# Optimization experiments

Measured on AMD Instinct MI355X. Metric: run time of the kernel, lower is better.

The kernel has to match this reference:

```python
import jax, jax.numpy as jnp
import numpy as np

N_HEAD = 16
D_MODEL = 1024
BATCH = 2
SEQ = 2048


def setup_inputs() -> dict:
    key = jax.random.key(0)
    ks = jax.random.split(key, 12)
    s = 0.02
    inp = {
        "q": jax.random.normal(ks[0], (BATCH, SEQ, D_MODEL), jnp.float32),
        "k": jax.random.normal(ks[1], (BATCH, SEQ, D_MODEL), jnp.float32),
        "v": jax.random.normal(ks[2], (BATCH, SEQ, D_MODEL), jnp.float32),
        "Wq": jax.random.normal(ks[3], (D_MODEL, D_MODEL), jnp.float32) * s,
        "bq": jnp.zeros((D_MODEL,), jnp.float32),
        "Wk": jax.random.normal(ks[4], (D_MODEL, D_MODEL), jnp.float32) * s,
        "bk": jnp.zeros((D_MODEL,), jnp.float32),
        "Wv": jax.random.normal(ks[5], (D_MODEL, D_MODEL), jnp.float32) * s,
        "bv": jnp.zeros((D_MODEL,), jnp.float32),
        "Wo": jax.random.normal(ks[6], (D_MODEL, D_MODEL), jnp.float32) * s,
        "bo": jnp.zeros((D_MODEL,), jnp.float32),
    }
    return inp


def reference(q, k, v, Wq, bq, Wk, bk, Wv, bv, Wo, bo):
    B, S, D = q.shape
    H = N_HEAD
    Dh = D // H
    # NOTE: faithful to source -- scale uses d_model, not head_dim
    scale = D ** 0.5

    # torch nn.Linear: y = x @ W.T + b
    qw = q @ Wq.T + bq
    kw = k @ Wk.T + bk
    vw = v @ Wv.T + bv

    # chunk(n_head, dim=-1) == contiguous last-dim head slices
    qh = qw.reshape(B, S, H, Dh)
    kh = kw.reshape(B, S, H, Dh)
    vh = vw.reshape(B, S, H, Dh)

    scores = jnp.einsum("bshd,bthd->bhst", qh, kh) / scale  # [B,H,S,S]
    causal = jnp.triu(jnp.ones((S, S), dtype=bool), k=1)
    scores = jnp.where(causal, -jnp.inf, scores)
    p = jax.nn.softmax(scores, axis=-1)
    out = jnp.einsum("bhst,bthd->bshd", p, vh).reshape(B, S, D)
    return out @ Wo.T + bo
```

## Files before the change

kernel.cpp:

```cpp
#include <hip/hip_runtime.h>
#include <hip/hip_bf16.h>
#include <stdint.h>
#include <type_traits>

#define NHEAD  16
#define DMODEL 1024
#define BATCH  2
#define SEQ    2048
#define DH     64
#define MROWS  (BATCH*SEQ)

typedef __attribute__((ext_vector_type(8))) short bf16x8;
typedef __attribute__((ext_vector_type(4))) float f32x4;

__device__ inline short f2bs(float f) {
    __hip_bfloat16 h = __float2bfloat16(f);
    return *reinterpret_cast<short*>(&h);
}

__device__ inline uint32_t pk2f(float lo, float hi) {
    uint32_t ul, uh;
    __builtin_memcpy(&ul, &lo, 4);
    __builtin_memcpy(&uh, &hi, 4);
    return __builtin_amdgcn_perm(uh + 0x8000u, ul + 0x8000u, 0x07060302u);
}

__device__ inline void async16(const void* g, void* l) {
    __builtin_amdgcn_global_load_lds(
        (__attribute__((address_space(1))) void*)g,
        (__attribute__((address_space(3))) void*)l, 16, 0, 0);
}

__global__ __launch_bounds__(256)
void convert_all(const float* __restrict__ Wq, const float* __restrict__ Wk,
                 const float* __restrict__ Wv, const float* __restrict__ Wo,
                 const float* __restrict__ q, const float* __restrict__ k,
                 const float* __restrict__ v,
                 __hip_bfloat16* __restrict__ Wqkv, __hip_bfloat16* __restrict__ Wob,
                 __hip_bfloat16* __restrict__ qb, __hip_bfloat16* __restrict__ kb,
                 __hip_bfloat16* __restrict__ vb)
{
    const int idx = (blockIdx.x * 256 + threadIdx.x) * 8;
    const float* src;
    __hip_bfloat16* dst;
    if (idx < 3 * 1048576) {
        const int g = idx >> 20;
        src = (g == 0 ? Wq : (g == 1 ? Wk : Wv)) + (idx & 1048575);
        dst = Wqkv + idx;
    } else if (idx < 4 * 1048576) {
        src = Wo + (idx - 3 * 1048576);
        dst = Wob + (idx - 3 * 1048576);
    } else if (idx < 8 * 1048576) {
        src = q + (idx - 4 * 1048576);
        dst = qb + (idx - 4 * 1048576);
    } else if (idx < 12 * 1048576) {
        src = k + (idx - 8 * 1048576);
        dst = kb + (idx - 8 * 1048576);
    } else {
        src = v + (idx - 12 * 1048576);
        dst = vb + (idx - 12 * 1048576);
    }
    float4 f0 = *(const float4*)src;
    float4 f1 = *(const float4*)(src + 4);
    short o[8];
    o[0] = f2bs(f0.x); o[1] = f2bs(f0.y); o[2] = f2bs(f0.z); o[3] = f2bs(f0.w);
    o[4] = f2bs(f1.x); o[5] = f2bs(f1.y); o[6] = f2bs(f1.z); o[7] = f2bs(f1.w);
    *(uint4*)dst = *(uint4*)o;
}

template <typename TC, bool DBUF, bool VTOUT>
__global__ __launch_bounds__(256, DBUF ? 2 : 3)
void gemm_bt(const __hip_bfloat16* __restrict__ A0, const __hip_bfloat16* __restrict__ A1,
             const __hip_bfloat16* __restrict__ A2,
             const __hip_bfloat16* __restrict__ B,
             const float* __restrict__ b0, const float* __restrict__ b1, const float* __restrict__ b2,
             TC* __restrict__ C0, TC* __restrict__ C1, TC* __restrict__ C2,
             float os0)
{
    __shared__ short As[DBUF ? 2 : 1][128 * 64];
    __shared__ short Bs[DBUF ? 2 : 1][128 * 64];

    const int t    = threadIdx.x;
    const int lane = t & 63;
    const int w    = t >> 6;
    const int wm   = (w >> 1) * 64;
    const int wn   = (w & 1) * 64;
    const int quad = lane >> 4;
    const int l16  = lane & 15;

    const int g = blockIdx.x >> 3;
    const __hip_bfloat16* A = (g == 0) ? A0 : (g == 1 ? A1 : A2);
    const float* bias       = (g == 0) ? b0 : (g == 1 ? b1 : b2);
    TC* C                   = (g == 0) ? C0 : (g == 1 ? C1 : C2);
    const float osc         = (g == 0) ? os0 : 1.f;
    const int    bm  = blockIdx.y * 128;
    const int    bnl = (blockIdx.x & 7) * 128;
    const size_t bng = (size_t)blockIdx.x * 128;

    f32x4 acc[4][4];
#pragma unroll
    for (int i = 0; i < 4; i++)
#pragma unroll
        for (int j = 0; j < 4; j++)
            acc[i][j] = (f32x4){0.f, 0.f, 0.f, 0.f};

    auto STAGEG = [&](int kt, int buf) {
#pragma unroll
        for (int i = 0; i < 4; i++) {
            const int p  = i * 256 + t;
            const int br = p >> 3;
            const int c8 = ((p & 7) - br) & 7;
            async16(B + (bng + br) * DMODEL + kt + c8 * 8,
                    &Bs[buf][(i * 256 + (w << 6)) * 8]);
            async16(A + (size_t)(bm + br) * DMODEL + kt + c8 * 8,
                    &As[buf][(i * 256 + (w << 6)) * 8]);
        }
    };

    int cur = 0;
    if constexpr (DBUF) STAGEG(0, 0);

    for (int kt = 0; kt < DMODEL; kt += 64) {
        __syncthreads();
        if constexpr (DBUF) {
            if (kt + 64 < DMODEL) STAGEG(kt + 64, cur ^ 1);
        } else {
            STAGEG(kt, 0);
            __syncthreads();
        }

#pragma unroll
        for (int kk = 0; kk < 2; kk++) {
            bf16x8 af[4], bf[4];
#pragma unroll
            for (int mi = 0; mi < 4; mi++) {
                const int row = wm + mi * 16 + l16;
                const int pc  = ((quad + 4 * kk) + row) & 7;
                af[mi] = *(const bf16x8*)&As[cur][row * 64 + pc * 8];
            }
#pragma unroll
            for (int ni = 0; ni < 4; ni++) {
                const int row = wn + ni * 16 + l16;
                const int pc  = ((quad + 4 * kk) + row) & 7;
                bf[ni] = *(const bf16x8*)&Bs[cur][row * 64 + pc * 8];
            }
#pragma unroll
            for (int mi = 0; mi < 4; mi++)
#pragma unroll
                for (int ni = 0; ni < 4; ni++)
                    acc[mi][ni] = __builtin_amdgcn_mfma_f32_16x16x32_bf16(
                        af[mi], bf[ni], acc[mi][ni], 0, 0, 0);
        }
        if constexpr (DBUF) cur ^= 1;
    }

#pragma unroll
    for (int mi = 0; mi < 4; mi++) {
#pragma unroll
        for (int ni = 0; ni < 4; ni++) {
            const int row0 = bm + wm + mi * 16 + quad * 4;
            const int coll = bnl + wn + ni * 16 + l16;
            const float bb = bias[coll];
            if (VTOUT && g == 2) {
                const int hh = coll >> 6, dd = coll & 63;
                const int bb_ = row0 >> 11, s0 = row0 & 2047;
                short o4[4];
#pragma unroll
                for (int r = 0; r < 4; r++) o4[r] = f2bs(acc[mi][ni][r] + bb);
                __hip_bfloat16* dst = (__hip_bfloat16*)C2 +
                    ((size_t)((bb_ * NHEAD + hh) * DH + dd)) * SEQ + s0;
                *(uint2*)dst = *(uint2*)o4;
            } else {
#pragma unroll
                for (int r = 0; r < 4; r++) {
                    const float val = (acc[mi][ni][r] + bb) * osc;
                    if constexpr (std::is_same<TC, float>::value)
                        C[(size_t)(row0 + r) * DMODEL + coll] = val;
                    else
                        C[(size_t)(row0 + r) * DMODEL + coll] = __float2bfloat16(val);
                }
            }
        }
    }
}

__global__ __launch_bounds__(256, 5)
void attn_flash_wg(const __hip_bfloat16* __restrict__ qp,
                   const __hip_bfloat16* __restrict__ kp,
                   const __hip_bfloat16* __restrict__ vt,
                   __hip_bfloat16* __restrict__ ao)
{
    __shared__ short Ks[2][64 * 64];
    __shared__ short Vs[2][64 * 64];

    const int t    = threadIdx.x;
    const int lane = t & 63;
    const int w    = t >> 6;
    const int l16  = lane & 15;
    const int quad = lane >> 4;

    const int bh = blockIdx.x & 31;
    const int p  = blockIdx.x >> 5;
    const int pa = p & 7, pb = p >> 3;
    const int st = (pb == 0) ? pa : (pb == 1) ? 15 - pa
                 : (pb == 2) ? 16 + pa : 31 - pa;
    const int b = bh >> 4;
    const int h = bh & 15;

    const __hip_bfloat16* qptr =
        qp + (size_t)(b * SEQ + 64 * st + 16 * w + l16) * DMODEL + h * DH + quad * 8;
    bf16x8 aq0 = *(const bf16x8*)qptr;
    bf16x8 aq1 = *(const bf16x8*)(qptr + 32);

    float l = 0.f;
    f32x4 oc[4];
#pragma unroll
    for (int dt = 0; dt < 4; dt++) oc[dt] = (f32x4){0.f, 0.f, 0.f, 0.f};

    const __hip_bfloat16* kbase = kp + (size_t)(b * SEQ) * DMODEL + h * DH;
    const __hip_bfloat16* vbase = vt + (size_t)(bh * DH) * SEQ;

    const int nst = st + 1;
    const int rql = 16 * w + l16;

    const int p1  = 256 + t;
    const int r0s = t >> 3,            r1s = p1 >> 3;
    const int c80 = ((t & 7) - r0s) & 7, c81 = ((p1 & 7) - r1s) & 7;
    const int kr0 = (r0s & 3) | ((r0s & 12) << 1) | ((r0s & 16) << 1) | ((r0s & 32) >> 3);
    const int kr1 = (r1s & 3) | ((r1s & 12) << 1) | ((r1s & 16) << 1) | ((r1s & 32) >> 3);
    const __hip_bfloat16* ks0 = kbase + (size_t)kr0 * DMODEL + c80 * 8;
    const __hip_bfloat16* ks1 = kbase + (size_t)kr1 * DMODEL + c81 * 8;
    const __hip_bfloat16* vs0 = vbase + (size_t)r0s * SEQ + c80 * 8;
    const __hip_bfloat16* vs1 = vbase + (size_t)r1s * SEQ + c81 * 8;

    const int d0 = ((w << 6)) * 8;
    const int d1 = (256 + (w << 6)) * 8;

    async16(ks0, &Ks[0][d0]);
    async16(ks1, &Ks[0][d1]);
    async16(vs0, &Vs[0][d0]);
    async16(vs1, &Vs[0][d1]);
    int cur = 0;
    int key0 = 0;

    for (int js = 0; js < nst; ++js) {
        __syncthreads();
        if (js + 1 < nst) {
            ks0 += (size_t)64 * DMODEL;  ks1 += (size_t)64 * DMODEL;
            vs0 += 64;                   vs1 += 64;
            const int nb = cur ^ 1;
            async16(ks0, &Ks[nb][d0]);
            async16(ks1, &Ks[nb][d1]);
            async16(vs0, &Vs[nb][d0]);
            async16(vs1, &Vs[nb][d1]);
        }

        f32x4 sc[4];
        __builtin_amdgcn_s_setprio(1);
#pragma unroll
        for (int ct = 0; ct < 4; ct++) {
            const int row = 16 * ct + l16;
            bf16x8 bk0 = *(const bf16x8*)&Ks[cur][row * 64 + ((quad + row) & 7) * 8];
            bf16x8 bk1 = *(const bf16x8*)&Ks[cur][row * 64 + ((quad + 4 + row) & 7) * 8];
            sc[ct] = __builtin_amdgcn_mfma_f32_16x16x32_bf16(
                bk0, aq0, (f32x4){0.f, 0.f, 0.f, 0.f}, 0, 0, 0);
            sc[ct] = __builtin_amdgcn_mfma_f32_16x16x32_bf16(bk1, aq1, sc[ct], 0, 0, 0);
        }
        __builtin_amdgcn_s_setprio(0);

        if (key0 == 64 * st) {
#pragma unroll
            for (int ct = 0; ct < 4; ct++)
#pragma unroll
                for (int r = 0; r < 4; r++) {
                    const int km = 8 * quad + 32 * (ct & 1) + 4 * (ct >> 1) + r;
                    if (km > rql) sc[ct][r] = -__builtin_inff();
                }
        }

        float psum = 0.f;
#pragma unroll
        for (int ct = 0; ct < 4; ct++)
#pragma unroll
            for (int r = 0; r < 4; r++) {
                const float e = exp2f(sc[ct][r]);
                sc[ct][r] = e;
                psum += e;
            }

        union U8 { uint32_t u[4]; bf16x8 v; } ap0u, ap1u;
        ap0u.u[0] = pk2f(sc[0][0], sc[0][1]);
        ap0u.u[1] = pk2f(sc[0][2], sc[0][3]);
        ap0u.u[2] = pk2f(sc[2][0], sc[2][1]);
        ap0u.u[3] = pk2f(sc[2][2], sc[2][3]);
        ap1u.u[0] = pk2f(sc[1][0], sc[1][1]);
        ap1u.u[1] = pk2f(sc[1][2], sc[1][3]);
        ap1u.u[2] = pk2f(sc[3][0], sc[3][1]);
        ap1u.u[3] = pk2f(sc[3][2], sc[3][3]);

        __builtin_amdgcn_s_setprio(1);
#pragma unroll
        for (int dt = 0; dt < 4; dt++) {
            const int row = 16 * dt + l16;
            bf16x8 bv0 = *(const bf16x8*)&Vs[cur][row * 64 + ((quad + row) & 7) * 8];
            bf16x8 bv1 = *(const bf16x8*)&Vs[cur][row * 64 + ((quad + 4 + row) & 7) * 8];
            oc[dt] = __builtin_amdgcn_mfma_f32_16x16x32_bf16(ap0u.v, bv0, oc[dt], 0, 0, 0);
            oc[dt] = __builtin_amdgcn_mfma_f32_16x16x32_bf16(ap1u.v, bv1, oc[dt], 0, 0, 0);
        }
        __builtin_amdgcn_s_setprio(0);

        psum += __shfl_xor(psum, 16);
        psum += __shfl_xor(psum, 32);
        l += psum;
        key0 += 64;
        cur ^= 1;
    }

    __hip_bfloat16* aobase = ao + (size_t)(b * SEQ + 64 * st + 16 * w) * DMODEL + h * DH;
#pragma unroll
    for (int r = 0; r < 4; r++) {
        const float lr  = __shfl(l, quad * 4 + r);
        const float inv = 1.f / lr;
        const int   row = quad * 4 + r;
#pragma unroll
        for (int dt = 0; dt < 4; dt++)
            aobase[(size_t)row * DMODEL + 16 * dt + l16] = __float2bfloat16(oc[dt][r] * inv);
    }
}

extern "C" void kernel_launch(void* const* d_in, const int* in_sizes, int n_in,
                              void* d_out, int out_size, void* d_ws, size_t ws_size,
                              hipStream_t stream) {
    const float* q  = (const float*)d_in[0];
    const float* k  = (const float*)d_in[1];
    const float* v  = (const float*)d_in[2];
    const float* Wq = (const float*)d_in[3];
    const float* bq = (const float*)d_in[4];
    const float* Wk = (const float*)d_in[5];
    const float* bk = (const float*)d_in[6];
    const float* Wv = (const float*)d_in[7];
    const float* bv = (const float*)d_in[8];
    const float* Wo = (const float*)d_in[9];
    const float* bo = (const float*)d_in[10];
    float* out = (float*)d_out;

    __hip_bfloat16* Wqkv = (__hip_bfloat16*)d_ws;
    __hip_bfloat16* Wob  = Wqkv + (size_t)3072 * 1024;
    __hip_bfloat16* qp   = Wob  + (size_t)1024 * 1024;
    __hip_bfloat16* kp   = qp   + (size_t)MROWS * DMODEL;
    __hip_bfloat16* vtg  = kp   + (size_t)MROWS * DMODEL;
    __hip_bfloat16* vb   = vtg  + (size_t)MROWS * DMODEL;
    __hip_bfloat16* qb   = (__hip_bfloat16*)d_out;
    __hip_bfloat16* kb   = qb + (size_t)MROWS * DMODEL;
    __hip_bfloat16* ao   = vb;

    const float qscale = 0.03125f * 1.44269504088896340736f;

    hipLaunchKernelGGL(convert_all, dim3(8192), dim3(256), 0, stream,
                       Wq, Wk, Wv, Wo, q, k, v, Wqkv, Wob, qb, kb, vb);

    hipLaunchKernelGGL((gemm_bt<__hip_bfloat16, false, true>), dim3(24, 32), dim3(256), 0, stream,
                       qb, kb, vb, Wqkv, bq, bk, bv, qp, kp, vtg, qscale);

    hipLaunchKernelGGL(attn_flash_wg, dim3(1024), dim3(256), 0, stream,
                       qp, kp, vtg, ao);

    hipLaunchKernelGGL((gemm_bt<float, true, false>), dim3(8, 32), dim3(256), 0, stream,
                       ao, ao, ao, Wob, bo, bo, bo, out, out, out, 1.0f);
}
```

Before: 211.3 us.

## Split long causal attention tiles across two blocks and add reduce kernel

Query tiles 16-31 of the causal attention now have their key range split in half across two workgroups. A static ordering table schedules the heaviest pieces first, and each split half writes unnormalized bf16 partial outputs plus row sums into scratch. A new attn_reduce2 kernel then combines the two halves and normalizes them. This balances load across the grid and shortens the tail of the longest tiles, at the cost of an extra launch and extra partial-result traffic. Separately, the fp32 output GEMM swaps its MFMA operands so each lane can store four contiguous columns as float4 with a vectorized bias load.

Result: no change. 208.4 us (-1.4%).

```diff
diff --git a/kernel.cpp b/kernel.cpp
--- a/kernel.cpp
+++ b/kernel.cpp
@@ -23,6 +23,13 @@
     __builtin_memcpy(&ul, &lo, 4);
     __builtin_memcpy(&uh, &hi, 4);
     return __builtin_amdgcn_perm(uh + 0x8000u, ul + 0x8000u, 0x07060302u);
+}
+
+__device__ inline float bs2f(short s) {
+    const uint32_t u = (uint32_t)(uint16_t)s << 16;
+    float f;
+    __builtin_memcpy(&f, &u, 4);
+    return f;
 }
 
 __device__ inline void async16(const void* g, void* l) {
@@ -77,6 +84,7 @@
              TC* __restrict__ C0, TC* __restrict__ C1, TC* __restrict__ C2,
              float os0)
 {
+    constexpr bool SWAPC = std::is_same<TC, float>::value;
     __shared__ short As[DBUF ? 2 : 1][128 * 64];
     __shared__ short Bs[DBUF ? 2 : 1][128 * 64];
 
@@ -147,9 +155,14 @@
 #pragma unroll
             for (int mi = 0; mi < 4; mi++)
 #pragma unroll
-                for (int ni = 0; ni < 4; ni++)
-                    acc[mi][ni] = __builtin_amdgcn_mfma_f32_16x16x32_bf16(
-                        af[mi], bf[ni], acc[mi][ni], 0, 0, 0);
+                for (int ni = 0; ni < 4; ni++) {
+                    if constexpr (SWAPC)
+                        acc[mi][ni] = __builtin_amdgcn_mfma_f32_16x16x32_bf16(
+                            bf[ni], af[mi], acc[mi][ni], 0, 0, 0);
+                    else
+                        acc[mi][ni] = __builtin_amdgcn_mfma_f32_16x16x32_bf16(
+                            af[mi], bf[ni], acc[mi][ni], 0, 0, 0);
+                }
         }
         if constexpr (DBUF) cur ^= 1;
     }
@@ -158,26 +171,35 @@
     for (int mi = 0; mi < 4; mi++) {
 #pragma unroll
         for (int ni = 0; ni < 4; ni++) {
-            const int row0 = bm + wm + mi * 16 + quad * 4;
-            const int coll = bnl + wn + ni * 16 + l16;
-            const float bb = bias[coll];
-            if (VTOUT && g == 2) {
-                const int hh = coll >> 6, dd = coll & 63;
-                const int bb_ = row0 >> 11, s0 = row0 & 2047;
-                short o4[4];
-#pragma unroll
-                for (int r = 0; r < 4; r++) o4[r] = f2bs(acc[mi][ni][r] + bb);
-                __hip_bfloat16* dst = (__hip_bfloat16*)C2 +
-                    ((size_t)((bb_ * NHEAD + hh) * DH + dd)) * SEQ + s0;
-                *(uint2*)dst = *(uint2*)o4;
+            if constexpr (SWAPC) {
+                const int m  = bm + wm + mi * 16 + l16;
+                const int nb = bnl + wn + ni * 16 + quad * 4;
+                const float4 b4 = *(const float4*)&bias[nb];
+                float4 o;
+                o.x = acc[mi][ni][0] + b4.x;
+                o.y = acc[mi][ni][1] + b4.y;
+                o.z = acc[mi][ni][2] + b4.z;
+                o.w = acc[mi][ni][3] + b4.w;
+                *(float4*)&C[(size_t)m * DMODEL + nb] = o;
             } else {
-#pragma unroll
-                for (int r = 0; r < 4; r++) {
-                    const float val = (acc[mi][ni][r] + bb) * osc;
-                    if constexpr (std::is_same<TC, float>::value)
-                        C[(size_t)(row0 + r) * DMODEL + coll] = val;
-                    else
+                const int row0 = bm + wm + mi * 16 + quad * 4;
+                const int coll = bnl + wn + ni * 16 + l16;
+                const float bb = bias[coll];
+                if (VTOUT && g == 2) {
+                    const int hh = coll >> 6, dd = coll & 63;
+                    const int bb_ = row0 >> 11, s0 = row0 & 2047;
+                    short o4[4];
+#pragma unroll
+                    for (int r = 0; r < 4; r++) o4[r] = f2bs(acc[mi][ni][r] + bb);
+                    __hip_bfloat16* dst = (__hip_bfloat16*)C2 +
+                        ((size_t)((bb_ * NHEAD + hh) * DH + dd)) * SEQ + s0;
+                    *(uint2*)dst = *(uint2*)o4;
+                } else {
+#pragma unroll
+                    for (int r = 0; r < 4; r++) {
+                        const float val = (acc[mi][ni][r] + bb) * osc;
                         C[(size_t)(row0 + r) * DMODEL + coll] = __float2bfloat16(val);
+                    }
                 }
             }
         }
@@ -188,8 +210,23 @@
 void attn_flash_wg(const __hip_bfloat16* __restrict__ qp,
                    const __hip_bfloat16* __restrict__ kp,
                    const __hip_bfloat16* __restrict__ vt,
-                   __hip_bfloat16* __restrict__ ao)
+                   __hip_bfloat16* __restrict__ ao,
+                   __hip_bfloat16* __restrict__ po,
+                   float* __restrict__ ml)
 {
+    static const unsigned char ord[48] = {
+        62, 63, 60, 15,
+        61, 58, 59, 56, 14,
+        57, 54, 55, 52, 13,
+        53, 50, 51, 48, 12,
+        49, 46, 47, 44, 11,
+        45, 42, 43, 40, 10,
+        41, 38, 39, 36,  9,
+        37, 34, 35, 32,  8,
+        33,  7,
+         6,  5,  4,  3,  2,  1,  0
+    };
+
     __shared__ short Ks[2][64 * 64];
     __shared__ short Vs[2][64 * 64];
 
@@ -200,10 +237,20 @@
     const int quad = lane >> 4;
 
     const int bh = blockIdx.x & 31;
-    const int p  = blockIdx.x >> 5;
-    const int pa = p & 7, pb = p >> 3;
-    const int st = (pb == 0) ? pa : (pb == 1) ? 15 - pa
-                 : (pb == 2) ? 16 + pa : 31 - pa;
+    const int u  = blockIdx.x >> 5;
+    const int v  = ord[u];
+    int st, js0, nst;
+    bool split;
+    if (v >= 32) {
+        st = v >> 1;
+        const int S  = st + 1;
+        const int h0 = (S + 1) >> 1;
+        if ((v & 1) == 0) { js0 = 0;  nst = h0; }
+        else              { js0 = h0; nst = S - h0; }
+        split = true;
+    } else {
+        st = v; js0 = 0; nst = st + 1; split = false;
+    }
     const int b = bh >> 4;
     const int h = bh & 15;
 
@@ -220,7 +267,6 @@
     const __hip_bfloat16* kbase = kp + (size_t)(b * SEQ) * DMODEL + h * DH;
     const __hip_bfloat16* vbase = vt + (size_t)(bh * DH) * SEQ;
 
-    const int nst = st + 1;
     const int rql = 16 * w + l16;
 
     const int p1  = 256 + t;
@@ -228,10 +274,11 @@
     const int c80 = ((t & 7) - r0s) & 7, c81 = ((p1 & 7) - r1s) & 7;
     const int kr0 = (r0s & 3) | ((r0s & 12) << 1) | ((r0s & 16) << 1) | ((r0s & 32) >> 3);
     const int kr1 = (r1s & 3) | ((r1s & 12) << 1) | ((r1s & 16) << 1) | ((r1s & 32) >> 3);
-    const __hip_bfloat16* ks0 = kbase + (size_t)kr0 * DMODEL + c80 * 8;
-    const __hip_bfloat16* ks1 = kbase + (size_t)kr1 * DMODEL + c81 * 8;
-    const __hip_bfloat16* vs0 = vbase + (size_t)r0s * SEQ + c80 * 8;
-    const __hip_bfloat16* vs1 = vbase + (size_t)r1s * SEQ + c81 * 8;
+    const int kofs = js0 * 64;
+    const __hip_bfloat16* ks0 = kbase + (size_t)(kofs + kr0) * DMODEL + c80 * 8;
+    const __hip_bfloat16* ks1 = kbase + (size_t)(kofs + kr1) * DMODEL + c81 * 8;
+    const __hip_bfloat16* vs0 = vbase + (size_t)r0s * SEQ + kofs + c80 * 8;
+    const __hip_bfloat16* vs1 = vbase + (size_t)r1s * SEQ + kofs + c81 * 8;
 
     const int d0 = ((w << 6)) * 8;
     const int d1 = (256 + (w << 6)) * 8;
@@ -241,7 +288,7 @@
     async16(vs0, &Vs[0][d0]);
     async16(vs1, &Vs[0][d1]);
     int cur = 0;
-    int key0 = 0;
+    int key0 = kofs;
 
     for (int js = 0; js < nst; ++js) {
         __syncthreads();
@@ -316,16 +363,59 @@
         cur ^= 1;
     }
 
-    __hip_bfloat16* aobase = ao + (size_t)(b * SEQ + 64 * st + 16 * w) * DMODEL + h * DH;
-#pragma unroll
-    for (int r = 0; r < 4; r++) {
-        const float lr  = __shfl(l, quad * 4 + r);
-        const float inv = 1.f / lr;
-        const int   row = quad * 4 + r;
-#pragma unroll
-        for (int dt = 0; dt < 4; dt++)
-            aobase[(size_t)row * DMODEL + 16 * dt + l16] = __float2bfloat16(oc[dt][r] * inv);
-    }
+    if (!split) {
+        __hip_bfloat16* aobase = ao + (size_t)(b * SEQ + 64 * st + 16 * w) * DMODEL + h * DH;
+#pragma unroll
+        for (int r = 0; r < 4; r++) {
+            const float lr  = __shfl(l, quad * 4 + r);
+            const float inv = 1.f / lr;
+            const int   row = quad * 4 + r;
+#pragma unroll
+            for (int dt = 0; dt < 4; dt++)
+                aobase[(size_t)row * DMODEL + 16 * dt + l16] =
+                    __float2bfloat16(oc[dt][r] * inv);
+        }
+    } else {
+        const int bid = ((v - 32) << 5) | bh;
+        __hip_bfloat16* pp = po + (size_t)bid * 4096;
+#pragma unroll
+        for (int r = 0; r < 4; r++) {
+            const int row = 16 * w + quad * 4 + r;
+#pragma unroll
+            for (int dt = 0; dt < 4; dt++)
+                pp[row * 64 + 16 * dt + l16] = __float2bfloat16(oc[dt][r]);
+        }
+        if (quad == 0)
+            ml[(size_t)bid * 64 + 16 * w + l16] = l;
+    }
+}
+
+__global__ __launch_bounds__(256)
+void attn_reduce2(const __hip_bfloat16* __restrict__ po, const float* __restrict__ ml,
+                  __hip_bfloat16* __restrict__ ao)
+{
+    const int t   = threadIdx.x;
+    const int rh  = blockIdx.x & 1;
+    const int bh  = (blockIdx.x >> 1) & 31;
+    const int k   = blockIdx.x >> 6;
+    const int st  = 16 + k;
+    const int bidA = ((2 * k) << 5) | bh;
+    const int bidB = ((2 * k + 1) << 5) | bh;
+    const int b   = bh >> 4;
+    const int h   = bh & 15;
+    const int row = rh * 32 + (t >> 3);
+    const int colg = (t & 7) * 8;
+
+    const float L = ml[(size_t)bidA * 64 + row] + ml[(size_t)bidB * 64 + row];
+    union { uint4 u; short s[8]; } pa, pb;
+    pa.u = *(const uint4*)&po[(size_t)bidA * 4096 + row * 64 + colg];
+    pb.u = *(const uint4*)&po[(size_t)bidB * 4096 + row * 64 + colg];
+    const float inv = 1.f / L;
+    short o8[8];
+#pragma unroll
+    for (int j = 0; j < 8; j++)
+        o8[j] = f2bs((bs2f(pa.s[j]) + bs2f(pb.s[j])) * inv);
+    *(uint4*)&ao[(size_t)(b * SEQ + 64 * st + row) * DMODEL + h * DH + colg] = *(uint4*)o8;
 }
 
 extern "C" void kernel_launch(void* const* d_in, const int* in_sizes, int n_in,
@@ -350,9 +440,11 @@
     __hip_bfloat16* kp   = qp   + (size_t)MROWS * DMODEL;
     __hip_bfloat16* vtg  = kp   + (size_t)MROWS * DMODEL;
     __hip_bfloat16* vb   = vtg  + (size_t)MROWS * DMODEL;
+    float*          mlb  = (float*)(vb + (size_t)MROWS * DMODEL);
     __hip_bfloat16* qb   = (__hip_bfloat16*)d_out;
     __hip_bfloat16* kb   = qb + (size_t)MROWS * DMODEL;
     __hip_bfloat16* ao   = vb;
+    __hip_bfloat16* po   = (__hip_bfloat16*)d_out;
 
     const float qscale = 0.03125f * 1.44269504088896340736f;
 
@@ -362,8 +454,11 @@
     hipLaunchKernelGGL((gemm_bt<__hip_bfloat16, false, true>), dim3(24, 32), dim3(256), 0, stream,
                        qb, kb, vb, Wqkv, bq, bk, bv, qp, kp, vtg, qscale);
 
-    hipLaunchKernelGGL(attn_flash_wg, dim3(1024), dim3(256), 0, stream,
-                       qp, kp, vtg, ao);
+    hipLaunchKernelGGL(attn_flash_wg, dim3(1536), dim3(256), 0, stream,
+                       qp, kp, vtg, ao, po, mlb);
+
+    hipLaunchKernelGGL(attn_reduce2, dim3(1024), dim3(256), 0, stream,
+                       po, mlb, ao);
 
     hipLaunchKernelGGL((gemm_bt<float, true, false>), dim3(8, 32), dim3(256), 0, stream,
                        ao, ao, ao, Wob, bo, bo, bo, out, out, out, 1.0f);
```
